# Kernel tuning notes

Hardware: AMD Instinct MI355X
Metric: run time of the kernel (lower is better)

Reference implementation:

```python
import jax, jax.numpy as jnp
import numpy as np

N_LEVELS = 16
N_FEATS = 2
MIN_RES = 16
MAX_RES = 2048
LOG2_T = 19
T = 1 << LOG2_T  # 524288 hash-table entries per level
B = np.exp((np.log(MAX_RES) - np.log(MIN_RES)) / (N_LEVELS - 1))  # per-level scale ~1.3819
PRIME_Y = np.uint32(2654435761)  # tcnn 2D spatial-hash prime (x prime is 1)
MASK = jnp.uint32(T - 1)


def hash_encode(uv, table):
    """Multiresolution hash-grid encoding (tcnn HashGrid, 2D, bilinear).
    uv: [N,2] in [0,1); table: [L,T,F]. Returns [N, L*F]."""
    outs = []
    for l in range(N_LEVELS):
        scale = MIN_RES * (B ** l) - 1.0          # tcnn grid_scale
        res = int(np.ceil(scale)) + 1             # tcnn grid_resolution
        dense = (res * res) <= T                  # small levels are dense grids
        pos = uv * jnp.float32(scale) + jnp.float32(0.5)
        pg_f = jnp.floor(pos)
        frac = pos - pg_f                          # [N,2] bilinear weights
        pg = pg_f.astype(jnp.uint32)

        def corner_idx(ox, oy):
            x = pg[:, 0] + jnp.uint32(ox)
            y = pg[:, 1] + jnp.uint32(oy)
            if dense:
                return (x + y * jnp.uint32(res)) & MASK
            return (x ^ (y * PRIME_Y)) & MASK

        fx = frac[:, 0:1]
        fy = frac[:, 1:2]
        tl = table[l]
        feat = ((1.0 - fx) * (1.0 - fy) * tl[corner_idx(0, 0)]
                + fx * (1.0 - fy) * tl[corner_idx(1, 0)]
                + (1.0 - fx) * fy * tl[corner_idx(0, 1)]
                + fx * fy * tl[corner_idx(1, 1)])
        outs.append(feat)
    return jnp.concatenate(outs, axis=-1)  # [N, 32]


def mlp(x, w0, w1, w2):
    # FullyFusedMLP: no biases, ReLU hidden, Sigmoid output
    h = jax.nn.relu(x @ w0)
    h = jax.nn.relu(h @ w1)
    return jax.nn.sigmoid(h @ w2)  # [N, 3]


def setup_inputs() -> dict:
    key = jax.random.key(0)
    ks = jax.random.split(key, 5)
    N = 2_097_152
    uv = jax.random.uniform(ks[0], (N, 2), jnp.float32)
    # tcnn HashGrid init: uniform in [-1e-4, 1e-4]
    table = jax.random.uniform(ks[1], (N_LEVELS, T, N_FEATS), jnp.float32, -1e-4, 1e-4)
    w0 = jax.random.normal(ks[2], (32, 64), jnp.float32) * jnp.float32(1.0 / np.sqrt(32))
    w1 = jax.random.normal(ks[3], (64, 64), jnp.float32) * jnp.float32(1.0 / np.sqrt(64))
    w2 = jax.random.normal(ks[4], (64, 3), jnp.float32) * jnp.float32(1.0 / np.sqrt(64))
    return {"uv": uv, "table": table, "w0": w0, "w1": w1, "w2": w2}


def reference(uv, table, w0, w1, w2):
    return mlp(hash_encode(uv, table), w0, w1, w2)
```

## Files before the change

kernel.cpp:

```cpp
#include <hip/hip_runtime.h>
#include <math.h>
#include <stdint.h>

#define NLV 16
#define LOG2T 19
#define TSZ (1u << LOG2T)
#define TMASK (TSZ - 1u)
#define PRIME_Y 2654435761u

#define NFRAG 14
#define WPF_USHORTS (NFRAG * 64 * 8)

#define NCOARSE 512
#define P1_PTS 8192
#define P2_CAP 5120

struct NGPParams {
    float scale[NLV];
    unsigned res[NLV];
    unsigned hashed_mask;
};

struct __align__(8) pairld { float x, y, z, w; };

typedef __attribute__((ext_vector_type(8))) short bf16x8;
typedef __attribute__((ext_vector_type(4))) float f32x4;

__device__ inline ushort bf16_rn(float f) {
    uint32_t u = __float_as_uint(f);
    return (ushort)((u + 0x7FFFu + ((u >> 16) & 1u)) >> 16);
}
__device__ inline uint32_t pack_bf16(float a, float b) {
    uint32_t ua = __float_as_uint(a);
    uint32_t ub = __float_as_uint(b);
    uint32_t lo = (ua + 0x7FFFu + ((ua >> 16) & 1u)) >> 16;
    uint32_t hi = (ub + 0x7FFFu + ((ub >> 16) & 1u)) & 0xFFFF0000u;
    return lo | hi;
}
__device__ inline uint32_t pack_trunc(float a, float b) {
    return __builtin_amdgcn_perm(__float_as_uint(a), __float_as_uint(b), 0x07060302u);
}
__device__ inline unsigned coarse_of(float2 v) {
    unsigned b = (unsigned)(v.y * 512.f); return b > 511u ? 511u : b;
}
__device__ inline unsigned fine_of(float2 v) {
    unsigned b = (unsigned)(v.x * 256.f); return b > 255u ? 255u : b;
}
__device__ inline int xcd_swz(int orig, int nwg) {
    const int q = nwg >> 3, r = nwg & 7;
    const int xcd = orig & 7, k = orig >> 3;
    return (xcd < r ? xcd * (q + 1) : r * (q + 1) + (xcd - r) * q) + k;
}

__global__ __launch_bounds__(256) void ngp_prep_wfrag(
    const float* __restrict__ w0, const float* __restrict__ w1,
    const float* __restrict__ w2, ushort* __restrict__ wpf)
{
    const int t = threadIdx.x;
    for (int i = 0; i < 4; ++i) {
        const int e = t + 256 * i;
        if (e >= NFRAG * 64) continue;
        const int f = e >> 6, lane = e & 63;
        const int g4 = lane >> 4, r16 = lane & 15;
        ushort v[8];
        if (f < 4) {
            const int n = f * 16 + r16, k0 = 8 * g4;
            #pragma unroll
            for (int j = 0; j < 8; ++j) v[j] = bf16_rn(w0[(k0 + j) * 64 + n]);
        } else if (f < 12) {
            const int q = f - 4;
            const int n = (q >> 1) * 16 + r16, k0 = (q & 1) * 32 + 8 * g4;
            #pragma unroll
            for (int j = 0; j < 8; ++j) v[j] = bf16_rn(w1[(k0 + j) * 64 + n]);
        } else {
            const int n = r16, k0 = (f - 12) * 32 + 8 * g4;
            #pragma unroll
            for (int j = 0; j < 8; ++j)
                v[j] = (n < 3) ? bf16_rn(w2[(k0 + j) * 3 + n]) : (ushort)0;
        }
        #pragma unroll
        for (int j = 0; j < 8; ++j) wpf[e * 8 + j] = v[j];
    }
}

__global__ __launch_bounds__(1024) void ngp_hist512(
    const float2* __restrict__ uv, uint32_t* __restrict__ hist, int n)
{
    __shared__ unsigned int h[NCOARSE];
    const int t = threadIdx.x;
    if (t < NCOARSE) h[t] = 0;
    __syncthreads();
    const int b0 = blockIdx.x * P1_PTS;
    #pragma unroll
    for (int k = 0; k < 8; ++k) {
        const int i = b0 + t + k * 1024;
        if (i < n) atomicAdd(&h[coarse_of(uv[i])], 1u);
    }
    __syncthreads();
    if (t < NCOARSE && h[t]) atomicAdd(&hist[t], h[t]);
}

__global__ __launch_bounds__(512) void ngp_scan512(
    const uint32_t* __restrict__ hist, uint32_t* __restrict__ base,
    uint32_t* __restrict__ cursor)
{
    __shared__ unsigned int s[NCOARSE];
    const int t = threadIdx.x;
    const uint32_t mine = hist[t];
    s[t] = mine;
    __syncthreads();
    for (int off = 1; off < NCOARSE; off <<= 1) {
        uint32_t v = (t >= off) ? s[t - off] : 0u;
        __syncthreads();
        s[t] += v;
        __syncthreads();
    }
    const uint32_t excl = s[t] - mine;
    base[t] = excl;
    cursor[t] = excl;
}

__global__ __launch_bounds__(1024) void ngp_pass1(
    const float2* __restrict__ uv, uint32_t* __restrict__ cursor,
    float2* __restrict__ suv, uint32_t* __restrict__ perm, int n)
{
    __shared__ float2       spt[P1_PTS];
    __shared__ unsigned int sid[P1_PTS];
    __shared__ unsigned int hist[NCOARSE], lbase[NCOARSE], lcur[NCOARSE], gbase[NCOARSE];
    __shared__ unsigned int stot;

    const int t = threadIdx.x;
    const int b0 = blockIdx.x * P1_PTS;
    if (t < NCOARSE) hist[t] = 0;
    __syncthreads();

    float2 p[8]; unsigned pc[8];
    #pragma unroll
    for (int k = 0; k < 8; ++k) {
        const int i = b0 + t + k * 1024;
        if (i < n) {
            p[k] = uv[i];
            pc[k] = coarse_of(p[k]);
            atomicAdd(&hist[pc[k]], 1u);
        } else pc[k] = 0xFFFFFFFFu;
    }
    __syncthreads();
    if (t < NCOARSE) lbase[t] = hist[t];
    __syncthreads();
    for (int off = 1; off < NCOARSE; off <<= 1) {
        uint32_t v = 0;
        if (t < NCOARSE && t >= off) v = lbase[t - off];
        __syncthreads();
        if (t < NCOARSE) lbase[t] += v;
        __syncthreads();
    }
    if (t < NCOARSE) {
        const uint32_t excl = lbase[t] - hist[t];
        lcur[t] = excl;
        gbase[t] = atomicAdd(&cursor[t], hist[t]);
        lbase[t] = excl;
        if (t == NCOARSE - 1) stot = excl + hist[t];
    }
    __syncthreads();
    #pragma unroll
    for (int k = 0; k < 8; ++k) {
        if (pc[k] != 0xFFFFFFFFu) {
            const uint32_t r = atomicAdd(&lcur[pc[k]], 1u);
            spt[r] = p[k];
            sid[r] = (unsigned)(b0 + t + k * 1024);
        }
    }
    __syncthreads();
    const uint32_t tot = stot;
    for (uint32_t j = t; j < tot; j += 1024) {
        const float2 v = spt[j];
        const unsigned c = coarse_of(v);
        const uint32_t d = gbase[c] + (j - lbase[c]);
        suv[d] = v;
        perm[d] = sid[j];
    }
}

__global__ __launch_bounds__(1024) void ngp_pass2(
    const uint32_t* __restrict__ basev, const uint32_t* __restrict__ histv,
    float2* __restrict__ suv, uint32_t* __restrict__ perm)
{
    __shared__ float2       spt[P2_CAP];
    __shared__ unsigned int sid[P2_CAP];
    __shared__ unsigned int hist[256], lbase[256], lcur[256];

    const int b = blockIdx.x;
    const uint32_t lo = basev[b];
    const uint32_t cnt = histv[b];
    if (cnt > P2_CAP) return;
    const int t = threadIdx.x;
    if (t < 256) hist[t] = 0;
    __syncthreads();
    for (uint32_t j = t; j < cnt; j += 1024) {
        const float2 v = suv[lo + j];
        spt[j] = v; sid[j] = perm[lo + j];
        atomicAdd(&hist[fine_of(v)], 1u);
    }
    __syncthreads();
    if (t < 256) lbase[t] = hist[t];
    __syncthreads();
    for (int off = 1; off < 256; off <<= 1) {
        uint32_t v = 0;
        if (t < 256 && t >= off) v = lbase[t - off];
        __syncthreads();
        if (t < 256) lbase[t] += v;
        __syncthreads();
    }
    if (t < 256) lcur[t] = lbase[t] - hist[t];
    __syncthreads();
    for (uint32_t j = t; j < cnt; j += 1024) {
        const float2 v = spt[j];
        const uint32_t r = atomicAdd(&lcur[fine_of(v)], 1u);
        suv[lo + r] = v;
        perm[lo + r] = sid[j];
    }
}

__global__ __launch_bounds__(256) void ngp_encode2_kernel(
    const float2* __restrict__ pts,
    const float2* __restrict__ table,
    uint32_t* __restrict__ xt,
    NGPParams p, int n, int chunks2)
{
    const int bid = blockIdx.x;
    const int pass = bid / chunks2;
    const int chunk = xcd_swz(bid - pass * chunks2, chunks2);
    const int base = chunk * 512 + threadIdx.x;

    float2 xy[2];
    #pragma unroll
    for (int q = 0; q < 2; ++q) {
        int idx = base + q * 256;
        xy[q] = pts[idx < n ? idx : (n - 1)];
    }

    const int l0 = (pass == 0) ? 0 : 9 + pass;
    const int l1 = (pass == 0) ? 9 : 9 + pass;

    for (int l = l0; l <= l1; ++l) {
        const float s = p.scale[l];
        const unsigned res = p.res[l];
        const bool hashed = (p.hashed_mask >> l) & 1u;
        const float2* tl = table + ((size_t)l << LOG2T);

        #pragma unroll
        for (int q = 0; q < 2; ++q) {
            const float px = xy[q].x * s + 0.5f;
            const float py = xy[q].y * s + 0.5f;
            const float fpx = floorf(px), fpy = floorf(py);
            const float fx = px - fpx, fy = py - fpy;
            const unsigned x0 = (unsigned)fpx, y0 = (unsigned)fpy;

            float2 c00, c10, c01, c11;
            if (!hashed) {
                const unsigned b0 = x0 + y0 * res;
                const pairld q0 = *(const pairld*)(tl + b0);
                const pairld q1 = *(const pairld*)(tl + b0 + res);
                c00 = make_float2(q0.x, q0.y); c10 = make_float2(q0.z, q0.w);
                c01 = make_float2(q1.x, q1.y); c11 = make_float2(q1.z, q1.w);
            } else {
                const unsigned hy0 = y0 * PRIME_Y;
                const unsigned hy1 = (y0 + 1u) * PRIME_Y;
                if (!(x0 & 1u)) {
                    const unsigned i0 = (x0 ^ hy0) & TMASK;
                    const unsigned i2 = (x0 ^ hy1) & TMASK;
                    const pairld q0 = *(const pairld*)(tl + (i0 & ~1u));
                    const pairld q2 = *(const pairld*)(tl + (i2 & ~1u));
                    if (i0 & 1u) { c00 = make_float2(q0.z, q0.w); c10 = make_float2(q0.x, q0.y); }
                    else         { c00 = make_float2(q0.x, q0.y); c10 = make_float2(q0.z, q0.w); }
                    if (i2 & 1u) { c01 = make_float2(q2.z, q2.w); c11 = make_float2(q2.x, q2.y); }
                    else         { c01 = make_float2(q2.x, q2.y); c11 = make_float2(q2.z, q2.w); }
                } else {
                    c00 = tl[(x0 ^ hy0) & TMASK];
                    c10 = tl[((x0 + 1u) ^ hy0) & TMASK];
                    c01 = tl[(x0 ^ hy1) & TMASK];
                    c11 = tl[((x0 + 1u) ^ hy1) & TMASK];
                }
            }

            const float w00 = (1.f - fx) * (1.f - fy);
            const float w10 = fx * (1.f - fy);
            const float w01 = (1.f - fx) * fy;
            const float w11 = fx * fy;
            const float f0 = w00 * c00.x + w10 * c10.x + w01 * c01.x + w11 * c11.x;
            const float f1 = w00 * c00.y + w10 * c10.y + w01 * c01.y + w11 * c11.y;
            const int idx = base + q * 256;
            if (idx < n) xt[(size_t)l * n + idx] = pack_bf16(f0, f1);
        }
    }
}

__global__ __launch_bounds__(256, 4) void ngp_mlp_persist(
    const uint32_t* __restrict__ xt,
    const ushort* __restrict__ wpf,
    const uint32_t* __restrict__ perm,
    float* __restrict__ out, int n, int nchunks)
{
    __shared__ __align__(16) ushort H[256 * 72];

    const int t = threadIdx.x;
    const int lane = t & 63;
    const int w = t >> 6;
    const int g4 = lane >> 4;
    const int r16 = lane & 15;

    bf16x8 wf[NFRAG];
    #pragma unroll
    for (int f = 0; f < NFRAG; ++f)
        wf[f] = *(const bf16x8*)(wpf + (size_t)(f * 64 + lane) * 8);

    for (int c = blockIdx.x; c < nchunks; c += gridDim.x) {
        const int pbase = c << 8;
        #pragma unroll
        for (int mi = 0; mi < 4; ++mi) {
            const int plocal = (w * 4 + mi) * 16 + r16;
            int pg = pbase + plocal;
            pg = pg < n ? pg : n - 1;
            union { uint32_t u[4]; bf16x8 v; } cv;
            #pragma unroll
            for (int c4 = 0; c4 < 4; ++c4)
                cv.u[c4] = xt[(size_t)(4 * g4 + c4) * n + pg];
            f32x4 a[4];
            #pragma unroll
            for (int nt = 0; nt < 4; ++nt)
                a[nt] = __builtin_amdgcn_mfma_f32_16x16x32_bf16(
                    wf[nt], cv.v, (f32x4){0.f, 0.f, 0.f, 0.f}, 0, 0, 0);
            const int pl = plocal * 72;
            #pragma unroll
            for (int nt = 0; nt < 4; ++nt) {
                const uint32_t d0 = pack_trunc(fmaxf(a[nt][1], 0.f), fmaxf(a[nt][0], 0.f));
                const uint32_t d1 = pack_trunc(fmaxf(a[nt][3], 0.f), fmaxf(a[nt][2], 0.f));
                *(uint2*)&H[pl + nt * 16 + 4 * g4] = make_uint2(d0, d1);
            }
        }
        #pragma unroll
        for (int mi = 0; mi < 4; ++mi) {
            const int plocal = (w * 4 + mi) * 16 + r16;
            const int pl = plocal * 72;
            const bf16x8 bh0 = *(const bf16x8*)&H[pl + 8 * g4];
            const bf16x8 bh1 = *(const bf16x8*)&H[pl + 32 + 8 * g4];
            #pragma unroll
            for (int nt = 0; nt < 4; ++nt) {
                f32x4 acc = __builtin_amdgcn_mfma_f32_16x16x32_bf16(
                    wf[4 + nt * 2], bh0, (f32x4){0.f, 0.f, 0.f, 0.f}, 0, 0, 0);
                acc = __builtin_amdgcn_mfma_f32_16x16x32_bf16(
                    wf[4 + nt * 2 + 1], bh1, acc, 0, 0, 0);
                const uint32_t d0 = pack_trunc(fmaxf(acc[1], 0.f), fmaxf(acc[0], 0.f));
                const uint32_t d1 = pack_trunc(fmaxf(acc[3], 0.f), fmaxf(acc[2], 0.f));
                *(uint2*)&H[pl + nt * 16 + 4 * g4] = make_uint2(d0, d1);
            }
            const bf16x8 ch0 = *(const bf16x8*)&H[pl + 8 * g4];
            const bf16x8 ch1 = *(const bf16x8*)&H[pl + 32 + 8 * g4];
            f32x4 z = __builtin_amdgcn_mfma_f32_16x16x32_bf16(
                wf[12], ch0, (f32x4){0.f, 0.f, 0.f, 0.f}, 0, 0, 0);
            z = __builtin_amdgcn_mfma_f32_16x16x32_bf16(wf[13], ch1, z, 0, 0, 0);
            if (g4 == 0) {
                const int pgs = pbase + plocal;
                if (pgs < n) {
                    const int pg = perm ? (int)perm[pgs] : pgs;
                    #pragma unroll
                    for (int r = 0; r < 3; ++r)
                        out[(size_t)pg * 3 + r] = 1.f / (1.f + __expf(-z[r]));
                }
            }
        }
    }
}

__global__ __launch_bounds__(256) void ngp_fused_kernel(
    const float2* __restrict__ uv,
    const float2* __restrict__ table,
    const float4* __restrict__ w0,
    const float4* __restrict__ w1,
    const float*  __restrict__ w2,
    float* __restrict__ out,
    NGPParams p, int n)
{
    __shared__ float4 sw0[512];
    __shared__ float4 sw1[1024];
    __shared__ float  sw2[192];
    const int t = threadIdx.x;
    #pragma unroll
    for (int i = 0; i < 2; i++) sw0[t + 256 * i] = w0[t + 256 * i];
    #pragma unroll
    for (int i = 0; i < 4; i++) sw1[t + 256 * i] = w1[t + 256 * i];
    if (t < 192) sw2[t] = w2[t];
    __syncthreads();
    const int gi = blockIdx.x * 256 + t;
    if (gi >= n) return;
    const float2 xy = uv[gi];
    float feat[32];
    #pragma unroll
    for (int l = 0; l < NLV; l++) {
        const float s = p.scale[l];
        const unsigned res = p.res[l];
        const float px = xy.x * s + 0.5f;
        const float py = xy.y * s + 0.5f;
        const float fpx = floorf(px), fpy = floorf(py);
        const float fx = px - fpx, fy = py - fpy;
        const unsigned x0 = (unsigned)fpx, y0 = (unsigned)fpy;
        unsigned i00, i10, i01, i11;
        if (!((p.hashed_mask >> l) & 1u)) {
            const unsigned b = x0 + y0 * res;
            i00 = b & TMASK; i10 = (b + 1u) & TMASK;
            i01 = (b + res) & TMASK; i11 = (b + res + 1u) & TMASK;
        } else {
            const unsigned hy0 = y0 * PRIME_Y;
            const unsigned hy1 = (y0 + 1u) * PRIME_Y;
            i00 = (x0 ^ hy0) & TMASK; i10 = ((x0 + 1u) ^ hy0) & TMASK;
            i01 = (x0 ^ hy1) & TMASK; i11 = ((x0 + 1u) ^ hy1) & TMASK;
        }
        const float2* tl = table + ((size_t)l << LOG2T);
        const float2 c00 = tl[i00], c10 = tl[i10], c01 = tl[i01], c11 = tl[i11];
        const float w00 = (1.f - fx) * (1.f - fy);
        const float w10 = fx * (1.f - fy);
        const float w01 = (1.f - fx) * fy;
        const float w11 = fx * fy;
        feat[2 * l]     = w00 * c00.x + w10 * c10.x + w01 * c01.x + w11 * c11.x;
        feat[2 * l + 1] = w00 * c00.y + w10 * c10.y + w01 * c01.y + w11 * c11.y;
    }
    float2 h0[32];
    #pragma unroll
    for (int j = 0; j < 32; j++) h0[j] = make_float2(0.f, 0.f);
    #pragma unroll
    for (int k = 0; k < 32; k++) {
        const float f = feat[k];
        #pragma unroll
        for (int j = 0; j < 16; j++) {
            const float4 ww = sw0[k * 16 + j];
            h0[2 * j].x = fmaf(f, ww.x, h0[2 * j].x);
            h0[2 * j].y = fmaf(f, ww.y, h0[2 * j].y);
            h0[2 * j + 1].x = fmaf(f, ww.z, h0[2 * j + 1].x);
            h0[2 * j + 1].y = fmaf(f, ww.w, h0[2 * j + 1].y);
        }
    }
    #pragma unroll
    for (int j = 0; j < 32; j++) {
        h0[j].x = fmaxf(h0[j].x, 0.f);
        h0[j].y = fmaxf(h0[j].y, 0.f);
    }
    float2 h1[32];
    #pragma unroll
    for (int j = 0; j < 32; j++) h1[j] = make_float2(0.f, 0.f);
    #pragma unroll
    for (int k = 0; k < 64; k++) {
        const float f = (k & 1) ? h0[k >> 1].y : h0[k >> 1].x;
        #pragma unroll
        for (int j = 0; j < 16; j++) {
            const float4 ww = sw1[k * 16 + j];
            h1[2 * j].x = fmaf(f, ww.x, h1[2 * j].x);
            h1[2 * j].y = fmaf(f, ww.y, h1[2 * j].y);
            h1[2 * j + 1].x = fmaf(f, ww.z, h1[2 * j + 1].x);
            h1[2 * j + 1].y = fmaf(f, ww.w, h1[2 * j + 1].y);
        }
    }
    #pragma unroll
    for (int j = 0; j < 32; j++) {
        h1[j].x = fmaxf(h1[j].x, 0.f);
        h1[j].y = fmaxf(h1[j].y, 0.f);
    }
    float z0 = 0.f, z1 = 0.f, z2 = 0.f;
    #pragma unroll
    for (int k = 0; k < 64; k++) {
        const float f = (k & 1) ? h1[k >> 1].y : h1[k >> 1].x;
        z0 = fmaf(f, sw2[3 * k + 0], z0);
        z1 = fmaf(f, sw2[3 * k + 1], z1);
        z2 = fmaf(f, sw2[3 * k + 2], z2);
    }
    out[3 * gi + 0] = 1.f / (1.f + __expf(-z0));
    out[3 * gi + 1] = 1.f / (1.f + __expf(-z1));
    out[3 * gi + 2] = 1.f / (1.f + __expf(-z2));
}

extern "C" void kernel_launch(void* const* d_in, const int* in_sizes, int n_in,
                              void* d_out, int out_size, void* d_ws, size_t ws_size,
                              hipStream_t stream) {
    const float2* uv    = (const float2*)d_in[0];
    const float2* table = (const float2*)d_in[1];
    const float*  w0f   = (const float*)d_in[2];
    const float*  w1f   = (const float*)d_in[3];
    const float*  w2f   = (const float*)d_in[4];
    float* out = (float*)d_out;

    const int n = in_sizes[0] / 2;

    NGPParams p;
    p.hashed_mask = 0;
    const double B = exp((log(2048.0) - log(16.0)) / 15.0);
    for (int l = 0; l < NLV; l++) {
        const double scale = 16.0 * pow(B, (double)l) - 1.0;
        const long long res = (long long)ceil(scale) + 1;
        p.scale[l] = (float)scale;
        p.res[l] = (unsigned)res;
        if (res * res > (long long)TSZ) p.hashed_mask |= (1u << l);
    }

    const size_t xt_bytes   = (size_t)NLV * (size_t)n * 4u;
    const size_t wpf_bytes  = ((size_t)WPF_USHORTS * 2u + 63u) & ~63ull;
    const size_t suv_bytes  = (size_t)n * 8u;
    const size_t perm_bytes = (size_t)n * 4u;
    const size_t ctl_bytes  = (size_t)NCOARSE * 4u * 3u;

    const size_t need_sorted = xt_bytes + wpf_bytes + suv_bytes + perm_bytes + ctl_bytes;
    const size_t need_plain  = xt_bytes + wpf_bytes;

    const int chunks  = (n + 255) / 256;
    const int chunks2 = (n + 511) / 512;

    if (ws_size < need_plain) {
        ngp_fused_kernel<<<chunks, 256, 0, stream>>>(
            uv, table, (const float4*)w0f, (const float4*)w1f, w2f, out, p, n);
        return;
    }

    uint32_t* xt  = (uint32_t*)d_ws;
    ushort*   wpf = (ushort*)((char*)d_ws + xt_bytes);
    ngp_prep_wfrag<<<1, 256, 0, stream>>>(w0f, w1f, w2f, wpf);

    const int mlp_blocks = chunks < 1024 ? chunks : 1024;

    if (ws_size < need_sorted) {
        ngp_encode2_kernel<<<7 * chunks2, 256, 0, stream>>>(uv, table, xt, p, n, chunks2);
        ngp_mlp_persist<<<mlp_blocks, 256, 0, stream>>>(xt, wpf, (const uint32_t*)nullptr, out, n, chunks);
        return;
    }

    float2*   suv    = (float2*)((char*)d_ws + xt_bytes + wpf_bytes);
    uint32_t* perm   = (uint32_t*)((char*)suv + suv_bytes);
    uint32_t* hist   = (uint32_t*)((char*)perm + perm_bytes);
    uint32_t* basev  = hist + NCOARSE;
    uint32_t* cursor = basev + NCOARSE;

    const int p1_blocks = (n + P1_PTS - 1) / P1_PTS;

    hipMemsetAsync(hist, 0, (size_t)NCOARSE * 4u, stream);
    ngp_hist512<<<p1_blocks, 1024, 0, stream>>>(uv, hist, n);
    ngp_scan512<<<1, NCOARSE, 0, stream>>>(hist, basev, cursor);
    ngp_pass1<<<p1_blocks, 1024, 0, stream>>>(uv, cursor, suv, perm, n);
    ngp_pass2<<<NCOARSE, 1024, 0, stream>>>(basev, hist, suv, perm);
    ngp_encode2_kernel<<<7 * chunks2, 256, 0, stream>>>(suv, table, xt, p, n, chunks2);
    ngp_mlp_persist<<<mlp_blocks, 256, 0, stream>>>(xt, wpf, perm, out, n, chunks);
}
```

Baseline: 191.6 us.

## Fuse dense-level encoding into MLP kernel, keep only hashed levels in staging buffer

Dense levels 0-11 are now interpolated directly inside the MLP kernel, with each lane group computing its four levels from the point coordinates. Only the four hashed levels 12-15 are precomputed by a separate encode kernel. This removes writing and rereading twelve levels of the bf16 feature buffer and shrinks the workspace. The MLP kernel also changes from a persistent grid to one block per chunk with XCD swizzling. In exchange the MLP kernel takes on gather latency and more register pressure, and per-level scale/res are passed through global memory.

```diff
diff --git a/kernel.cpp b/kernel.cpp
--- a/kernel.cpp
+++ b/kernel.cpp
@@ -7,6 +7,7 @@
 #define TSZ (1u << LOG2T)
 #define TMASK (TSZ - 1u)
 #define PRIME_Y 2654435761u
+#define NHASH 4
 
 #define NFRAG 14
 #define WPF_USHORTS (NFRAG * 64 * 8)
@@ -54,9 +55,11 @@
 
 __global__ __launch_bounds__(256) void ngp_prep_wfrag(
     const float* __restrict__ w0, const float* __restrict__ w1,
-    const float* __restrict__ w2, ushort* __restrict__ wpf)
-{
-    const int t = threadIdx.x;
+    const float* __restrict__ w2, ushort* __restrict__ wpf,
+    float* __restrict__ gscale, unsigned* __restrict__ gres, NGPParams p)
+{
+    const int t = threadIdx.x;
+    if (t < NLV) { gscale[t] = p.scale[t]; gres[t] = p.res[t]; }
     for (int i = 0; i < 4; ++i) {
         const int e = t + 256 * i;
         if (e >= NFRAG * 64) continue;
@@ -221,7 +224,7 @@
     }
 }
 
-__global__ __launch_bounds__(256) void ngp_encode2_kernel(
+__global__ __launch_bounds__(256) void ngp_encode_hashed(
     const float2* __restrict__ pts,
     const float2* __restrict__ table,
     uint32_t* __restrict__ xt,
@@ -239,65 +242,55 @@
         xy[q] = pts[idx < n ? idx : (n - 1)];
     }
 
-    const int l0 = (pass == 0) ? 0 : 9 + pass;
-    const int l1 = (pass == 0) ? 9 : 9 + pass;
-
-    for (int l = l0; l <= l1; ++l) {
-        const float s = p.scale[l];
-        const unsigned res = p.res[l];
-        const bool hashed = (p.hashed_mask >> l) & 1u;
-        const float2* tl = table + ((size_t)l << LOG2T);
-
-        #pragma unroll
-        for (int q = 0; q < 2; ++q) {
-            const float px = xy[q].x * s + 0.5f;
-            const float py = xy[q].y * s + 0.5f;
-            const float fpx = floorf(px), fpy = floorf(py);
-            const float fx = px - fpx, fy = py - fpy;
-            const unsigned x0 = (unsigned)fpx, y0 = (unsigned)fpy;
-
-            float2 c00, c10, c01, c11;
-            if (!hashed) {
-                const unsigned b0 = x0 + y0 * res;
-                const pairld q0 = *(const pairld*)(tl + b0);
-                const pairld q1 = *(const pairld*)(tl + b0 + res);
-                c00 = make_float2(q0.x, q0.y); c10 = make_float2(q0.z, q0.w);
-                c01 = make_float2(q1.x, q1.y); c11 = make_float2(q1.z, q1.w);
-            } else {
-                const unsigned hy0 = y0 * PRIME_Y;
-                const unsigned hy1 = (y0 + 1u) * PRIME_Y;
-                if (!(x0 & 1u)) {
-                    const unsigned i0 = (x0 ^ hy0) & TMASK;
-                    const unsigned i2 = (x0 ^ hy1) & TMASK;
-                    const pairld q0 = *(const pairld*)(tl + (i0 & ~1u));
-                    const pairld q2 = *(const pairld*)(tl + (i2 & ~1u));
-                    if (i0 & 1u) { c00 = make_float2(q0.z, q0.w); c10 = make_float2(q0.x, q0.y); }
-                    else         { c00 = make_float2(q0.x, q0.y); c10 = make_float2(q0.z, q0.w); }
-                    if (i2 & 1u) { c01 = make_float2(q2.z, q2.w); c11 = make_float2(q2.x, q2.y); }
-                    else         { c01 = make_float2(q2.x, q2.y); c11 = make_float2(q2.z, q2.w); }
-                } else {
-                    c00 = tl[(x0 ^ hy0) & TMASK];
-                    c10 = tl[((x0 + 1u) ^ hy0) & TMASK];
-                    c01 = tl[(x0 ^ hy1) & TMASK];
-                    c11 = tl[((x0 + 1u) ^ hy1) & TMASK];
-                }
-            }
-
-            const float w00 = (1.f - fx) * (1.f - fy);
-            const float w10 = fx * (1.f - fy);
-            const float w01 = (1.f - fx) * fy;
-            const float w11 = fx * fy;
-            const float f0 = w00 * c00.x + w10 * c10.x + w01 * c01.x + w11 * c11.x;
-            const float f1 = w00 * c00.y + w10 * c10.y + w01 * c01.y + w11 * c11.y;
-            const int idx = base + q * 256;
-            if (idx < n) xt[(size_t)l * n + idx] = pack_bf16(f0, f1);
-        }
-    }
-}
-
-__global__ __launch_bounds__(256, 4) void ngp_mlp_persist(
+    const int l = 12 + pass;
+    const float s = p.scale[l];
+    const float2* tl = table + ((size_t)l << LOG2T);
+
+    #pragma unroll
+    for (int q = 0; q < 2; ++q) {
+        const float px = xy[q].x * s + 0.5f;
+        const float py = xy[q].y * s + 0.5f;
+        const float fpx = floorf(px), fpy = floorf(py);
+        const float fx = px - fpx, fy = py - fpy;
+        const unsigned x0 = (unsigned)fpx, y0 = (unsigned)fpy;
+
+        float2 c00, c10, c01, c11;
+        const unsigned hy0 = y0 * PRIME_Y;
+        const unsigned hy1 = (y0 + 1u) * PRIME_Y;
+        if (!(x0 & 1u)) {
+            const unsigned i0 = (x0 ^ hy0) & TMASK;
+            const unsigned i2 = (x0 ^ hy1) & TMASK;
+            const pairld q0 = *(const pairld*)(tl + (i0 & ~1u));
+            const pairld q2 = *(const pairld*)(tl + (i2 & ~1u));
+            if (i0 & 1u) { c00 = make_float2(q0.z, q0.w); c10 = make_float2(q0.x, q0.y); }
+            else         { c00 = make_float2(q0.x, q0.y); c10 = make_float2(q0.z, q0.w); }
+            if (i2 & 1u) { c01 = make_float2(q2.z, q2.w); c11 = make_float2(q2.x, q2.y); }
+            else         { c01 = make_float2(q2.x, q2.y); c11 = make_float2(q2.z, q2.w); }
+        } else {
+            c00 = tl[(x0 ^ hy0) & TMASK];
+            c10 = tl[((x0 + 1u) ^ hy0) & TMASK];
+            c01 = tl[(x0 ^ hy1) & TMASK];
+            c11 = tl[((x0 + 1u) ^ hy1) & TMASK];
+        }
+
+        const float w00 = (1.f - fx) * (1.f - fy);
+        const float w10 = fx * (1.f - fy);
+        const float w01 = (1.f - fx) * fy;
+        const float w11 = fx * fy;
+        const float f0 = w00 * c00.x + w10 * c10.x + w01 * c01.x + w11 * c11.x;
+        const float f1 = w00 * c00.y + w10 * c10.y + w01 * c01.y + w11 * c11.y;
+        const int idx = base + q * 256;
+        if (idx < n) xt[(size_t)pass * n + idx] = pack_bf16(f0, f1);
+    }
+}
+
+__global__ __launch_bounds__(256, 4) void ngp_mlp_fused(
+    const float2* __restrict__ pts,
+    const float2* __restrict__ table,
     const uint32_t* __restrict__ xt,
     const ushort* __restrict__ wpf,
+    const float* __restrict__ gscale,
+    const unsigned* __restrict__ gres,
     const uint32_t* __restrict__ perm,
     float* __restrict__ out, int n, int nchunks)
 {
@@ -314,59 +307,93 @@
     for (int f = 0; f < NFRAG; ++f)
         wf[f] = *(const bf16x8*)(wpf + (size_t)(f * 64 + lane) * 8);
 
-    for (int c = blockIdx.x; c < nchunks; c += gridDim.x) {
-        const int pbase = c << 8;
-        #pragma unroll
-        for (int mi = 0; mi < 4; ++mi) {
-            const int plocal = (w * 4 + mi) * 16 + r16;
-            int pg = pbase + plocal;
-            pg = pg < n ? pg : n - 1;
-            union { uint32_t u[4]; bf16x8 v; } cv;
+    float lsc[4]; unsigned lrs[4]; const float2* ltb[4];
+    #pragma unroll
+    for (int c = 0; c < 4; ++c) {
+        const int lv = 4 * g4 + c;
+        const int lvc = lv < 12 ? lv : 0;
+        lsc[c] = gscale[lvc];
+        lrs[c] = gres[lvc];
+        ltb[c] = table + ((size_t)lvc << LOG2T);
+    }
+
+    const int c = xcd_swz(blockIdx.x, nchunks);
+    const int pbase = c << 8;
+
+    #pragma unroll
+    for (int mi = 0; mi < 4; ++mi) {
+        const int plocal = (w * 4 + mi) * 16 + r16;
+        int pg = pbase + plocal;
+        pg = pg < n ? pg : n - 1;
+        union { uint32_t u[4]; bf16x8 v; } cv;
+        if (g4 == 3) {
             #pragma unroll
             for (int c4 = 0; c4 < 4; ++c4)
-                cv.u[c4] = xt[(size_t)(4 * g4 + c4) * n + pg];
-            f32x4 a[4];
+                cv.u[c4] = xt[(size_t)c4 * n + pg];
+        } else {
+            const float2 ptv = pts[pg];
             #pragma unroll
-            for (int nt = 0; nt < 4; ++nt)
-                a[nt] = __builtin_amdgcn_mfma_f32_16x16x32_bf16(
-                    wf[nt], cv.v, (f32x4){0.f, 0.f, 0.f, 0.f}, 0, 0, 0);
-            const int pl = plocal * 72;
-            #pragma unroll
-            for (int nt = 0; nt < 4; ++nt) {
-                const uint32_t d0 = pack_trunc(fmaxf(a[nt][1], 0.f), fmaxf(a[nt][0], 0.f));
-                const uint32_t d1 = pack_trunc(fmaxf(a[nt][3], 0.f), fmaxf(a[nt][2], 0.f));
-                *(uint2*)&H[pl + nt * 16 + 4 * g4] = make_uint2(d0, d1);
+            for (int c4 = 0; c4 < 4; ++c4) {
+                const float s = lsc[c4];
+                const unsigned res = lrs[c4];
+                const float px = ptv.x * s + 0.5f;
+                const float py = ptv.y * s + 0.5f;
+                const float fpx = floorf(px), fpy = floorf(py);
+                const float fx = px - fpx, fy = py - fpy;
+                const unsigned x0 = (unsigned)fpx, y0 = (unsigned)fpy;
+                const unsigned b0 = x0 + y0 * res;
+                const pairld q0 = *(const pairld*)(ltb[c4] + b0);
+                const pairld q1 = *(const pairld*)(ltb[c4] + b0 + res);
+                const float w00 = (1.f - fx) * (1.f - fy);
+                const float w10 = fx * (1.f - fy);
+                const float w01 = (1.f - fx) * fy;
+                const float w11 = fx * fy;
+                const float f0 = w00 * q0.x + w10 * q0.z + w01 * q1.x + w11 * q1.z;
+                const float f1 = w00 * q0.y + w10 * q0.w + w01 * q1.y + w11 * q1.w;
+                cv.u[c4] = pack_bf16(f0, f1);
             }
         }
+        f32x4 a[4];
         #pragma unroll
-        for (int mi = 0; mi < 4; ++mi) {
-            const int plocal = (w * 4 + mi) * 16 + r16;
-            const int pl = plocal * 72;
-            const bf16x8 bh0 = *(const bf16x8*)&H[pl + 8 * g4];
-            const bf16x8 bh1 = *(const bf16x8*)&H[pl + 32 + 8 * g4];
-            #pragma unroll
-            for (int nt = 0; nt < 4; ++nt) {
-                f32x4 acc = __builtin_amdgcn_mfma_f32_16x16x32_bf16(
-                    wf[4 + nt * 2], bh0, (f32x4){0.f, 0.f, 0.f, 0.f}, 0, 0, 0);
-                acc = __builtin_amdgcn_mfma_f32_16x16x32_bf16(
-                    wf[4 + nt * 2 + 1], bh1, acc, 0, 0, 0);
-                const uint32_t d0 = pack_trunc(fmaxf(acc[1], 0.f), fmaxf(acc[0], 0.f));
-                const uint32_t d1 = pack_trunc(fmaxf(acc[3], 0.f), fmaxf(acc[2], 0.f));
-                *(uint2*)&H[pl + nt * 16 + 4 * g4] = make_uint2(d0, d1);
-            }
-            const bf16x8 ch0 = *(const bf16x8*)&H[pl + 8 * g4];
-            const bf16x8 ch1 = *(const bf16x8*)&H[pl + 32 + 8 * g4];
-            f32x4 z = __builtin_amdgcn_mfma_f32_16x16x32_bf16(
-                wf[12], ch0, (f32x4){0.f, 0.f, 0.f, 0.f}, 0, 0, 0);
-            z = __builtin_amdgcn_mfma_f32_16x16x32_bf16(wf[13], ch1, z, 0, 0, 0);
-            if (g4 == 0) {
-                const int pgs = pbase + plocal;
-                if (pgs < n) {
-                    const int pg = perm ? (int)perm[pgs] : pgs;
-                    #pragma unroll
-                    for (int r = 0; r < 3; ++r)
-                        out[(size_t)pg * 3 + r] = 1.f / (1.f + __expf(-z[r]));
-                }
+        for (int nt = 0; nt < 4; ++nt)
+            a[nt] = __builtin_amdgcn_mfma_f32_16x16x32_bf16(
+                wf[nt], cv.v, (f32x4){0.f, 0.f, 0.f, 0.f}, 0, 0, 0);
+        const int pl = plocal * 72;
+        #pragma unroll
+        for (int nt = 0; nt < 4; ++nt) {
+            const uint32_t d0 = pack_trunc(fmaxf(a[nt][1], 0.f), fmaxf(a[nt][0], 0.f));
+            const uint32_t d1 = pack_trunc(fmaxf(a[nt][3], 0.f), fmaxf(a[nt][2], 0.f));
+            *(uint2*)&H[pl + nt * 16 + 4 * g4] = make_uint2(d0, d1);
+        }
+    }
+    #pragma unroll
+    for (int mi = 0; mi < 4; ++mi) {
+        const int plocal = (w * 4 + mi) * 16 + r16;
+        const int pl = plocal * 72;
+        const bf16x8 bh0 = *(const bf16x8*)&H[pl + 8 * g4];
+        const bf16x8 bh1 = *(const bf16x8*)&H[pl + 32 + 8 * g4];
+        #pragma unroll
+        for (int nt = 0; nt < 4; ++nt) {
+            f32x4 acc = __builtin_amdgcn_mfma_f32_16x16x32_bf16(
+                wf[4 + nt * 2], bh0, (f32x4){0.f, 0.f, 0.f, 0.f}, 0, 0, 0);
+            acc = __builtin_amdgcn_mfma_f32_16x16x32_bf16(
+                wf[4 + nt * 2 + 1], bh1, acc, 0, 0, 0);
+            const uint32_t d0 = pack_trunc(fmaxf(acc[1], 0.f), fmaxf(acc[0], 0.f));
+            const uint32_t d1 = pack_trunc(fmaxf(acc[3], 0.f), fmaxf(acc[2], 0.f));
+            *(uint2*)&H[pl + nt * 16 + 4 * g4] = make_uint2(d0, d1);
+        }
+        const bf16x8 ch0 = *(const bf16x8*)&H[pl + 8 * g4];
+        const bf16x8 ch1 = *(const bf16x8*)&H[pl + 32 + 8 * g4];
+        f32x4 z = __builtin_amdgcn_mfma_f32_16x16x32_bf16(
+            wf[12], ch0, (f32x4){0.f, 0.f, 0.f, 0.f}, 0, 0, 0);
+        z = __builtin_amdgcn_mfma_f32_16x16x32_bf16(wf[13], ch1, z, 0, 0, 0);
+        if (g4 == 0) {
+            const int pgs = pbase + plocal;
+            if (pgs < n) {
+                const int pg = perm ? (int)perm[pgs] : pgs;
+                #pragma unroll
+                for (int r = 0; r < 3; ++r)
+                    out[(size_t)pg * 3 + r] = 1.f / (1.f + __expf(-z[r]));
             }
         }
     }
@@ -500,8 +527,8 @@
         if (res * res > (long long)TSZ) p.hashed_mask |= (1u << l);
     }
 
-    const size_t xt_bytes   = (size_t)NLV * (size_t)n * 4u;
-    const size_t wpf_bytes  = ((size_t)WPF_USHORTS * 2u + 63u) & ~63ull;
+    const size_t xt_bytes   = (size_t)NHASH * (size_t)n * 4u;
+    const size_t wpf_bytes  = ((size_t)WPF_USHORTS * 2u + 256u + 63u) & ~63ull;
     const size_t suv_bytes  = (size_t)n * 8u;
     const size_t perm_bytes = (size_t)n * 4u;
     const size_t ctl_bytes  = (size_t)NCOARSE * 4u * 3u;
@@ -518,15 +545,16 @@
         return;
     }
 
-    uint32_t* xt  = (uint32_t*)d_ws;
-    ushort*   wpf = (ushort*)((char*)d_ws + xt_bytes);
-    ngp_prep_wfrag<<<1, 256, 0, stream>>>(w0f, w1f, w2f, wpf);
-
-    const int mlp_blocks = chunks < 1024 ? chunks : 1024;
+    uint32_t* xt     = (uint32_t*)d_ws;
+    ushort*   wpf    = (ushort*)((char*)d_ws + xt_bytes);
+    float*    gscale = (float*)((char*)wpf + WPF_USHORTS * 2u);
+    unsigned* gres   = (unsigned*)(gscale + NLV);
+    ngp_prep_wfrag<<<1, 256, 0, stream>>>(w0f, w1f, w2f, wpf, gscale, gres, p);
 
     if (ws_size < need_sorted) {
-        ngp_encode2_kernel<<<7 * chunks2, 256, 0, stream>>>(uv, table, xt, p, n, chunks2);
-        ngp_mlp_persist<<<mlp_blocks, 256, 0, stream>>>(xt, wpf, (const uint32_t*)nullptr, out, n, chunks);
+        ngp_encode_hashed<<<NHASH * chunks2, 256, 0, stream>>>(uv, table, xt, p, n, chunks2);
+        ngp_mlp_fused<<<chunks, 256, 0, stream>>>(uv, table, xt, wpf, gscale, gres,
+                                                  (const uint32_t*)nullptr, out, n, chunks);
         return;
     }
 
@@ -543,6 +571,7 @@
     ngp_scan512<<<1, NCOARSE, 0, stream>>>(hist, basev, cursor);
     ngp_pass1<<<p1_blocks, 1024, 0, stream>>>(uv, cursor, suv, perm, n);
     ngp_pass2<<<NCOARSE, 1024, 0, stream>>>(basev, hist, suv, perm);
-    ngp_encode2_kernel<<<7 * chunks2, 256, 0, stream>>>(suv, table, xt, p, n, chunks2);
-    ngp_mlp_persist<<<mlp_blocks, 256, 0, stream>>>(xt, wpf, perm, out, n, chunks);
-}
+    ngp_encode_hashed<<<NHASH * chunks2, 256, 0, stream>>>(suv, table, xt, p, n, chunks2);
+    ngp_mlp_fused<<<chunks, 256, 0, stream>>>(suv, table, xt, wpf, gscale, gres,
+                                              perm, out, n, chunks);
+}
```

Result: slower. 196.7 us (+2.7%).
